# Optimization experiments

Measured on AMD Instinct MI355X. Metric: run time of the kernel, lower is better.

## Reference

```python
import jax, jax.numpy as jnp
import numpy as np

BN_EPS = 1e-5


def setup_inputs() -> dict:
    key = jax.random.key(0)
    ks = jax.random.split(key, 8)
    B, C, H, W_ = 64, 512, 28, 28
    return {
        "x": jax.random.normal(ks[0], (B, C, H, W_), dtype=jnp.float32),
        "rsign_bias": 0.1 * jax.random.normal(ks[1], (C,), dtype=jnp.float32),
        "W": jax.random.normal(ks[2], (C, C), dtype=jnp.float32) * 0.05,  # 1x1 conv weight [out,in]
        "bn_gamma": jnp.ones((C,), dtype=jnp.float32),
        "bn_beta": jnp.zeros((C,), dtype=jnp.float32),
        "bn_mean": 0.1 * jax.random.normal(ks[3], (C,), dtype=jnp.float32),
        "bn_var": jax.random.uniform(ks[4], (C,), dtype=jnp.float32, minval=0.5, maxval=1.5),
        "pr_slope": jax.random.uniform(ks[5], (C,), dtype=jnp.float32, minval=0.1, maxval=0.35),
        "pr_shift": 0.1 * jax.random.normal(ks[6], (C,), dtype=jnp.float32),
        "pr_bias": 0.1 * jax.random.normal(ks[7], (C,), dtype=jnp.float32),
    }


def reference(x, rsign_bias, W, bn_gamma, bn_beta, bn_mean, bn_var,
              pr_slope, pr_shift, pr_bias):
    # x: [B, C, H, W] (NCHW). All params are per-channel [C] except W: [C_out, C_in].
    c = lambda v: v[None, :, None, None]  # broadcast per-channel over NCHW

    # RSign: learnable per-channel shift then binarize (forward = sign)
    a = jnp.sign(x + c(rsign_bias))

    # scaled_sign 1x1 conv: per-output-channel scale = mean(|W|), binarized weight
    scale = jnp.mean(jnp.abs(W), axis=1)          # [C_out]
    Wb = jnp.sign(W) * scale[:, None]             # [C_out, C_in]
    y = jnp.einsum('bchw,oc->bohw', a, Wb)        # 1x1 conv == channel GEMM

    # BatchNorm2d (inference form with running stats)
    bn = c(bn_gamma) * (y - c(bn_mean)) * jax.lax.rsqrt(c(bn_var) + BN_EPS) + c(bn_beta)

    # residual shortcut
    s = bn + x

    # RPReLU: prelu(x - shift) + bias, per-channel learnable slope/shift/bias
    t = s - c(pr_shift)
    out = jnp.where(t > 0, t, c(pr_slope) * t) + c(pr_bias)
    return out
```

## Files before the change

kernel.cpp:

```cpp
#include <hip/hip_runtime.h>
#include <cstdint>

#define C_     512
#define HW_    784
#define B_     64
#define BN_EPS 1e-5f


__global__ __launch_bounds__(64) void precompute_kernel(
    const float* __restrict__ W,
    const float* __restrict__ bn_gamma, const float* __restrict__ bn_beta,
    const float* __restrict__ bn_mean,  const float* __restrict__ bn_var,
    const float* __restrict__ pr_slope, const float* __restrict__ pr_shift,
    const float* __restrict__ pr_bias,
    uint32_t* __restrict__ wbits, float4* __restrict__ params)
{
    const int o    = blockIdx.x;
    const int lane = threadIdx.x;
    const float4* wrow4 = (const float4*)(W + (size_t)o * C_);
    const float4 u = wrow4[2 * lane];
    const float4 v = wrow4[2 * lane + 1];

    float s = fabsf(u.x) + fabsf(u.y) + fabsf(u.z) + fabsf(u.w)
            + fabsf(v.x) + fabsf(v.y) + fabsf(v.z) + fabsf(v.w);
    for (int off = 32; off > 0; off >>= 1) s += __shfl_down(s, off, 64);

    uint32_t m8 = (u.x < 0.f ? 1u : 0u)  | (u.y < 0.f ? 2u : 0u)
                | (u.z < 0.f ? 4u : 0u)  | (u.w < 0.f ? 8u : 0u)
                | (v.x < 0.f ? 16u : 0u) | (v.y < 0.f ? 32u : 0u)
                | (v.z < 0.f ? 64u : 0u) | (v.w < 0.f ? 128u : 0u);

    const uint32_t g0 = __shfl(m8, 4 * lane + 0, 64);
    const uint32_t g1 = __shfl(m8, 4 * lane + 1, 64);
    const uint32_t g2 = __shfl(m8, 4 * lane + 2, 64);
    const uint32_t g3 = __shfl(m8, 4 * lane + 3, 64);
    if (lane < 16)
        wbits[o * 16 + lane] = g0 | (g1 << 8) | (g2 << 16) | (g3 << 24);

    if (lane == 0) {
        float scale = s * (1.0f / (float)C_);
        float r  = rsqrtf(bn_var[o] + BN_EPS);
        float A  = bn_gamma[o] * scale * r;
        float A2 = -2.0f * A;
        float C2 = (float)C_ * A + bn_beta[o] - bn_gamma[o] * bn_mean[o] * r
                 - pr_shift[o];
        params[o] = make_float4(A2, C2, pr_slope[o], pr_bias[o]);
    }
}

__global__ __launch_bounds__(1024, 4) void fused_kernel(
    const float* __restrict__ x, const float* __restrict__ rsign_bias,
    const uint32_t* __restrict__ wbits, const float4* __restrict__ params,
    float* __restrict__ out)
{
    __shared__ uint32_t abits[64 * 17];
    __shared__ float    xlds[16][32][64];

    const int i  = threadIdx.x;
    const int jj = __builtin_amdgcn_readfirstlane(threadIdx.y);

    const uint32_t pair = (uint32_t)blockIdx.x * 64u + (uint32_t)i;
    const uint32_t b    = pair / 784u;
    const uint32_t hw   = pair - b * 784u;
    const size_t   base = (size_t)b * (C_ * HW_) + hw;
    const float*   xg   = x + base;

    const int c0 = jj * 32;

    {
        float v[32];
        #pragma unroll
        for (int t = 0; t < 32; ++t)
            v[t] = xg[(size_t)(c0 + t) * HW_];

        uint32_t m = 0;
        #pragma unroll
        for (int t = 0; t < 32; ++t) {
            xlds[jj][t][i] = v[t];
            if (v[t] + rsign_bias[c0 + t] < 0.f) m |= (1u << t);
        }
        abits[i * 17 + jj] = m;
    }
    __syncthreads();

    uint32_t a[16];
    #pragma unroll
    for (int w = 0; w < 16; ++w) a[w] = abits[i * 17 + w];

    float* og = out + base;

    #pragma unroll
    for (int oo = 0; oo < 32; ++oo) {
        const int o = c0 + oo;
        const uint32_t* wr = wbits + o * 16;
        int P = 0;
        #pragma unroll
        for (int w = 0; w < 16; ++w) P += __popc(a[w] ^ wr[w]);

        const float4 p = params[o];
        const float t = fmaf(p.x, (float)P, p.y + xlds[jj][oo][i]);
        const float r = fmaf(p.z, fminf(t, 0.f), fmaxf(t, 0.f) + p.w);
        og[(size_t)o * HW_] = r;
    }
}

extern "C" void kernel_launch(void* const* d_in, const int* in_sizes, int n_in,
                              void* d_out, int out_size, void* d_ws, size_t ws_size,
                              hipStream_t stream) {
    const float* x          = (const float*)d_in[0];
    const float* rsign_bias = (const float*)d_in[1];
    const float* W          = (const float*)d_in[2];
    const float* bn_gamma   = (const float*)d_in[3];
    const float* bn_beta    = (const float*)d_in[4];
    const float* bn_mean    = (const float*)d_in[5];
    const float* bn_var     = (const float*)d_in[6];
    const float* pr_slope   = (const float*)d_in[7];
    const float* pr_shift   = (const float*)d_in[8];
    const float* pr_bias    = (const float*)d_in[9];
    float* out = (float*)d_out;

    uint32_t* wbits  = (uint32_t*)d_ws;
    float4*   params = (float4*)((char*)d_ws + 32768);

    precompute_kernel<<<dim3(C_), dim3(64), 0, stream>>>(
        W, bn_gamma, bn_beta, bn_mean, bn_var, pr_slope, pr_shift, pr_bias,
        wbits, params);

    fused_kernel<<<dim3(784), dim3(64, 16), 0, stream>>>(
        x, rsign_bias, wbits, params, out);
}
```

Measured before the change: 243.1 us.

## Process two pixels per thread with float2 I/O and drop LDS x staging

Each thread now handles two adjacent spatial positions, loading x and storing out as float2, and computes two popcount sums that share each weight-bit load. The 32 KB shared-memory copy of x is removed: the residual value is re-read from global memory (expected to hit in cache) in the output loop. Grid size is halved and launch bounds raised to 8 blocks per CU to allow more occupancy now that LDS use is small. The trade-off is more registers per thread for two activation-bit sets, and a second global read of x that relies on cache hits.

```diff
diff --git a/kernel.cpp b/kernel.cpp
--- a/kernel.cpp
+++ b/kernel.cpp
@@ -3,6 +3,7 @@
 
 #define C_     512
 #define HW_    784
+#define HW2_   392
 #define B_     64
 #define BN_EPS 1e-5f
 
@@ -48,59 +49,70 @@
     }
 }
 
-__global__ __launch_bounds__(1024, 4) void fused_kernel(
+__global__ __launch_bounds__(1024, 8) void fused_kernel(
     const float* __restrict__ x, const float* __restrict__ rsign_bias,
     const uint32_t* __restrict__ wbits, const float4* __restrict__ params,
     float* __restrict__ out)
 {
-    __shared__ uint32_t abits[64 * 17];
-    __shared__ float    xlds[16][32][64];
+    __shared__ uint32_t abits0[64 * 17];
+    __shared__ uint32_t abits1[64 * 17];
 
     const int i  = threadIdx.x;
     const int jj = __builtin_amdgcn_readfirstlane(threadIdx.y);
 
-    const uint32_t pair = (uint32_t)blockIdx.x * 64u + (uint32_t)i;
-    const uint32_t b    = pair / 784u;
-    const uint32_t hw   = pair - b * 784u;
-    const size_t   base = (size_t)b * (C_ * HW_) + hw;
-    const float*   xg   = x + base;
+    const uint32_t duo = (uint32_t)blockIdx.x * 64u + (uint32_t)i;
+    const uint32_t b   = duo / 392u;
+    const uint32_t hw2 = duo - b * 392u;
+    const float2* xg = (const float2*)x   + (size_t)b * (C_ * HW2_) + hw2;
+    float2*       og = (float2*)out       + (size_t)b * (C_ * HW2_) + hw2;
 
     const int c0 = jj * 32;
 
     {
-        float v[32];
+        float2 v[32];
         #pragma unroll
         for (int t = 0; t < 32; ++t)
-            v[t] = xg[(size_t)(c0 + t) * HW_];
+            v[t] = xg[(size_t)(c0 + t) * HW2_];
 
-        uint32_t m = 0;
+        uint32_t m0 = 0, m1 = 0;
         #pragma unroll
         for (int t = 0; t < 32; ++t) {
-            xlds[jj][t][i] = v[t];
-            if (v[t] + rsign_bias[c0 + t] < 0.f) m |= (1u << t);
+            const float rb = rsign_bias[c0 + t];
+            if (v[t].x + rb < 0.f) m0 |= (1u << t);
+            if (v[t].y + rb < 0.f) m1 |= (1u << t);
         }
-        abits[i * 17 + jj] = m;
+        abits0[i * 17 + jj] = m0;
+        abits1[i * 17 + jj] = m1;
     }
     __syncthreads();
 
-    uint32_t a[16];
+    uint32_t a0[16], a1[16];
     #pragma unroll
-    for (int w = 0; w < 16; ++w) a[w] = abits[i * 17 + w];
-
-    float* og = out + base;
+    for (int w = 0; w < 16; ++w) {
+        a0[w] = abits0[i * 17 + w];
+        a1[w] = abits1[i * 17 + w];
+    }
 
     #pragma unroll
     for (int oo = 0; oo < 32; ++oo) {
         const int o = c0 + oo;
         const uint32_t* wr = wbits + o * 16;
-        int P = 0;
+        int P0 = 0, P1 = 0;
         #pragma unroll
-        for (int w = 0; w < 16; ++w) P += __popc(a[w] ^ wr[w]);
+        for (int w = 0; w < 16; ++w) {
+            const uint32_t q = wr[w];
+            P0 += __popc(a0[w] ^ q);
+            P1 += __popc(a1[w] ^ q);
+        }
 
         const float4 p = params[o];
-        const float t = fmaf(p.x, (float)P, p.y + xlds[jj][oo][i]);
-        const float r = fmaf(p.z, fminf(t, 0.f), fmaxf(t, 0.f) + p.w);
-        og[(size_t)o * HW_] = r;
+        const float2 xr = xg[(size_t)o * HW2_];
+        const float t0 = fmaf(p.x, (float)P0, p.y + xr.x);
+        const float t1 = fmaf(p.x, (float)P1, p.y + xr.y);
+        float2 r;
+        r.x = fmaf(p.z, fminf(t0, 0.f), fmaxf(t0, 0.f) + p.w);
+        r.y = fmaf(p.z, fminf(t1, 0.f), fmaxf(t1, 0.f) + p.w);
+        og[(size_t)o * HW2_] = r;
     }
 }
 
@@ -126,6 +138,6 @@
         W, bn_gamma, bn_beta, bn_mean, bn_var, pr_slope, pr_shift, pr_bias,
         wbits, params);
 
-    fused_kernel<<<dim3(784), dim3(64, 16), 0, stream>>>(
+    fused_kernel<<<dim3(392), dim3(64, 16), 0, stream>>>(
         x, rsign_bias, wbits, params, out);
 }
```

After: 330.2 us. 1.36x slower.
